# Kernel tuning notes

Hardware: AMD Instinct MI355X
Metric: run time of the kernel (lower is better)

## Reference

```python
import jax, jax.numpy as jnp
import numpy as np

C, K, D = 256, 16, 256  # clusters, cluster_size, embed_dim
MARGIN = 1.0
EPS = 1e-6  # torch pairwise_distance eps


def setup_inputs() -> dict:
    key = jax.random.key(0)
    batch = jax.random.normal(key, (C, K, D), dtype=jnp.float32)
    return {"batch": batch}


def reference(batch):
    # world_size == 1, rank == 0  ->  my_embeds == all_embeds
    c, k, d = batch.shape
    emb = batch.reshape(-1, d)                       # [N, D], N = c*k
    n = emb.shape[0]

    sq = jnp.sum(emb * emb, axis=-1)                 # [N]
    d2 = sq[:, None] + sq[None, :] - 2.0 * (emb @ emb.T)
    dist = jnp.sqrt(jnp.maximum(d2, 0.0))            # [N, N]

    labels = jnp.repeat(jnp.arange(c), k)            # [N]
    pos_mask = labels[:, None] == labels[None, :]    # [N, N]

    # hardest positive: masked max (masked entries -> -1, matching pytorch code)
    pos_idx = jnp.argmax(jnp.where(pos_mask, dist, -1.0), axis=1)
    # hardest negative: masked min (positives -> +inf)
    neg_idx = jnp.argmin(jnp.where(pos_mask, jnp.inf, dist), axis=1)

    positives = emb[pos_idx]                         # [N, D]
    negatives = emb[neg_idx]                         # [N, D]

    # TripletMarginLoss(margin=1.0, p=2): pairwise_distance adds eps to the diff
    d_ap = jnp.linalg.norm(emb - positives + EPS, axis=-1)
    d_an = jnp.linalg.norm(emb - negatives + EPS, axis=-1)
    loss = jnp.mean(jnp.maximum(d_ap - d_an + MARGIN, 0.0))
    return loss
```

## Files before the change

### kernel.cpp

```cpp
#include <hip/hip_runtime.h>
#include <math.h>

#define CC 256
#define KK 16
#define DD 256
#define NN 4096
#define EPSV 1e-6f

typedef unsigned long long u64;
typedef __attribute__((ext_vector_type(8))) short short8v;
typedef __attribute__((ext_vector_type(8))) unsigned short ushort8v;
typedef __attribute__((ext_vector_type(4))) float f32x4;

__global__ __launch_bounds__(256) void prep_kernel(const float* __restrict__ emb,
                                                   float* __restrict__ sq,
                                                   unsigned short* __restrict__ hi,
                                                   u64* __restrict__ posk,
                                                   u64* __restrict__ negk,
                                                   float* __restrict__ out) {
  __shared__ __attribute__((aligned(16))) unsigned short hiS[16][264];
  const int g = blockIdx.x;
  const int t = threadIdx.x;
  const int r = t >> 4, q = t & 15;
  const int row = g * 16 + r;

  const float* src = emb + (size_t)row * DD + q * 16;
  float s = 0.f;
  #pragma unroll
  for (int i = 0; i < 4; ++i) {
    float4 v = *reinterpret_cast<const float4*>(src + 4 * i);
    float f[4] = {v.x, v.y, v.z, v.w};
    #pragma unroll
    for (int e = 0; e < 4; ++e) {
      s += f[e] * f[e];
      hiS[r][q * 16 + 4 * i + e] = (unsigned short)(__float_as_uint(f[e]) >> 16);
    }
  }
  #pragma unroll
  for (int off = 1; off < 16; off <<= 1) s += __shfl_xor(s, off);
  if (q == 0) {
    sq[row] = s;
    posk[row] = 0ull;
    negk[row] = ~0ull;
  }
  if (g == 0 && t == 0) out[0] = 0.0f;
  __syncthreads();

  #pragma unroll
  for (int h = 0; h < 2; ++h) {
    int q2 = h * 256 + t;
    int s2 = q2 >> 6, fl = q2 & 63;
    int col = 32 * s2 + 8 * (fl >> 4);
    ushort8v hv = *reinterpret_cast<const ushort8v*>(&hiS[fl & 15][col]);
    *reinterpret_cast<ushort8v*>(hi + ((size_t)(g * 8 + s2) * 64 + fl) * 8) = hv;
  }
}

__device__ __forceinline__ void gll16(const unsigned short* g, unsigned short* l) {
  __builtin_amdgcn_global_load_lds(
      (const __attribute__((address_space(1))) unsigned int*)(const void*)g,
      (__attribute__((address_space(3))) unsigned int*)(void*)l, 16, 0, 0);
}

__global__ __launch_bounds__(256, 2) void mine_mfma_kernel(const unsigned short* __restrict__ hi,
                                                           const float* __restrict__ sq,
                                                           u64* __restrict__ posk,
                                                           u64* __restrict__ negk) {
  __shared__ __attribute__((aligned(16))) unsigned short ldsB[8][4096];

  const int bid = blockIdx.x;
  const int wg = (bid & 7) * 128 + (bid >> 3);
  const int ib = wg >> 5, jb = wg & 31;
  const bool diag = (ib == jb);
  const int ibRow = ib * 128, jbRow = jb * 128;

  const int tid = threadIdx.x;
  const int lane = tid & 63;
  const int w = tid >> 6;
  const int fr = lane & 15;
  const int grp = lane >> 4;

  {
    const int c0 = 2 * w, c1 = c0 + 1;
    const unsigned short* g0 = hi + ((size_t)(jb * 8 + c0) * 8) * 512 + lane * 8;
    const unsigned short* g1 = hi + ((size_t)(jb * 8 + c1) * 8) * 512 + lane * 8;
    #pragma unroll
    for (int s = 0; s < 8; ++s) {
      gll16(g0 + s * 512, &ldsB[s][c0 * 512]);
      gll16(g1 + s * 512, &ldsB[s][c1 * 512]);
    }
  }
  short8v a[8][2];
  #pragma unroll
  for (int m = 0; m < 2; ++m) {
    const unsigned short* ga = hi + ((size_t)(ib * 8 + 2 * w + m) * 8) * 512 + lane * 8;
    #pragma unroll
    for (int s = 0; s < 8; ++s)
      a[s][m] = *reinterpret_cast<const short8v*>(ga + s * 512);
  }
  __syncthreads();

  f32x4 acc[2][8];
  #pragma unroll
  for (int m = 0; m < 2; ++m)
    #pragma unroll
    for (int n = 0; n < 8; ++n)
      acc[m][n] = (f32x4){0.f, 0.f, 0.f, 0.f};

  #pragma unroll
  for (int s = 0; s < 8; ++s) {
    short8v b[8];
    #pragma unroll
    for (int n = 0; n < 8; ++n)
      b[n] = *reinterpret_cast<const short8v*>(&ldsB[s][n * 512 + lane * 8]);
    #pragma unroll
    for (int m = 0; m < 2; ++m)
      #pragma unroll
      for (int n = 0; n < 8; ++n)
        acc[m][n] = __builtin_amdgcn_mfma_f32_16x16x32_bf16(a[s][m], b[n], acc[m][n], 0, 0, 0);
  }

  float sqjv[8]; int jglob[8];
  #pragma unroll
  for (int n = 0; n < 8; ++n) {
    jglob[n] = jbRow + n * 16 + fr;
    sqjv[n] = sq[jglob[n]];
  }

  #pragma unroll
  for (int m = 0; m < 2; ++m) {
    #pragma unroll
    for (int r = 0; r < 4; ++r) {
      const int gi = ibRow + w * 32 + m * 16 + grp * 4 + r;
      const float sqiv = sq[gi];
      float pv = -1.0f; int pj = -1;
      float nv = 3.0e38f; int nj = 0x7fffffff;
      #pragma unroll
      for (int n = 0; n < 8; ++n) {
        const float d2 = fmaxf(sqiv + sqjv[n] - 2.0f * acc[m][n][r], 0.0f);
        const int j = jglob[n];
        const bool isPos = diag && ((j >> 4) == (gi >> 4));
        if (isPos) {
          if (d2 > pv || (d2 == pv && j < pj)) { pv = d2; pj = j; }
        } else {
          if (d2 < nv || (d2 == nv && j < nj)) { nv = d2; nj = j; }
        }
      }
      #pragma unroll
      for (int off = 1; off < 16; off <<= 1) {
        float ov = __shfl_xor(nv, off); int oj = __shfl_xor(nj, off);
        if (ov < nv || (ov == nv && oj < nj)) { nv = ov; nj = oj; }
        float pov = __shfl_xor(pv, off); int poj = __shfl_xor(pj, off);
        if (pov > pv || (pov == pv && ((unsigned)poj < (unsigned)pj))) { pv = pov; pj = poj; }
      }
      if (fr == 0) {
        if (nj != 0x7fffffff)
          atomicMin(&negk[gi], ((u64)__float_as_uint(nv) << 32) | (unsigned)nj);
        if (diag && pj >= 0)
          atomicMax(&posk[gi], ((u64)__float_as_uint(pv) << 32) |
                                   (unsigned)(0xFFFFFFFFu - (unsigned)pj));
      }
    }
  }
}

__global__ __launch_bounds__(1024) void triplet_kernel(const float* __restrict__ emb,
                                                       const u64* __restrict__ posk,
                                                       const u64* __restrict__ negk,
                                                       float* __restrict__ out) {
  __shared__ float part[16];
  const int w = threadIdx.x >> 6;
  const int lane = threadIdx.x & 63;
  const int i = blockIdx.x * 16 + w;

  u64 pk = posk[i], nk = negk[i];
  int p = (int)(0xFFFFFFFFu - (unsigned)(pk & 0xFFFFFFFFu));
  int nidx = (int)(nk & 0xFFFFFFFFu);

  float4 e  = *reinterpret_cast<const float4*>(emb + (size_t)i * DD + 4 * lane);
  float4 ep = *reinterpret_cast<const float4*>(emb + (size_t)p * DD + 4 * lane);
  float4 en = *reinterpret_cast<const float4*>(emb + (size_t)nidx * DD + 4 * lane);

  float dpx = e.x - ep.x + EPSV, dpy = e.y - ep.y + EPSV,
        dpz = e.z - ep.z + EPSV, dpw = e.w - ep.w + EPSV;
  float dnx = e.x - en.x + EPSV, dny = e.y - en.y + EPSV,
        dnz = e.z - en.z + EPSV, dnw = e.w - en.w + EPSV;
  float sp = dpx * dpx + dpy * dpy + dpz * dpz + dpw * dpw;
  float sn = dnx * dnx + dny * dny + dnz * dnz + dnw * dnw;
  #pragma unroll
  for (int off = 32; off; off >>= 1) {
    sp += __shfl_xor(sp, off);
    sn += __shfl_xor(sn, off);
  }
  if (lane == 0) part[w] = fmaxf(sqrtf(sp) - sqrtf(sn) + 1.0f, 0.0f);
  __syncthreads();
  if (threadIdx.x == 0) {
    float s = 0.f;
    #pragma unroll
    for (int k = 0; k < 16; ++k) s += part[k];
    atomicAdd(out, s * (1.0f / NN));
  }
}

extern "C" void kernel_launch(void* const* d_in, const int* in_sizes, int n_in,
                              void* d_out, int out_size, void* d_ws, size_t ws_size,
                              hipStream_t stream) {
  const float* emb = (const float*)d_in[0];
  char* ws = (char*)d_ws;
  float* sq = (float*)ws;
  u64* posk = (u64*)(ws + (16 << 10));
  u64* negk = (u64*)(ws + (48 << 10));
  unsigned short* hi = (unsigned short*)(ws + (96 << 10));
  float* out = (float*)d_out;

  prep_kernel<<<256, 256, 0, stream>>>(emb, sq, hi, posk, negk, out);
  mine_mfma_kernel<<<1024, 256, 0, stream>>>(hi, sq, posk, negk);
  triplet_kernel<<<256, 1024, 0, stream>>>(emb, posk, negk, out);
}
```

Baseline: 96.40 us.

## Fuse prep, mining and triplet stages into one cooperative kernel with grid syncs

Replaces the three separate launches (prep, MFMA mining, triplet loss) with a single cooperative kernel of 256 blocks of 512 threads, separated by grid-wide syncs. The mining tile is enlarged to 256x256 per block, processed in two 128-column halves, so each row keeps its running argmax/argmin in registers and issues fewer atomics. The aim is to remove launch gaps and atomic traffic, at the cost of fewer, larger blocks (lower occupancy and parallelism) and grid-sync overhead.

```diff
diff --git a/kernel.cpp b/kernel.cpp
--- a/kernel.cpp
+++ b/kernel.cpp
@@ -1,8 +1,9 @@
 #include <hip/hip_runtime.h>
+#include <hip/hip_cooperative_groups.h>
 #include <math.h>
 
-#define CC 256
-#define KK 16
+namespace cg = cooperative_groups;
+
 #define DD 256
 #define NN 4096
 #define EPSV 1e-6f
@@ -11,50 +12,6 @@
 typedef __attribute__((ext_vector_type(8))) short short8v;
 typedef __attribute__((ext_vector_type(8))) unsigned short ushort8v;
 typedef __attribute__((ext_vector_type(4))) float f32x4;
-
-__global__ __launch_bounds__(256) void prep_kernel(const float* __restrict__ emb,
-                                                   float* __restrict__ sq,
-                                                   unsigned short* __restrict__ hi,
-                                                   u64* __restrict__ posk,
-                                                   u64* __restrict__ negk,
-                                                   float* __restrict__ out) {
-  __shared__ __attribute__((aligned(16))) unsigned short hiS[16][264];
-  const int g = blockIdx.x;
-  const int t = threadIdx.x;
-  const int r = t >> 4, q = t & 15;
-  const int row = g * 16 + r;
-
-  const float* src = emb + (size_t)row * DD + q * 16;
-  float s = 0.f;
-  #pragma unroll
-  for (int i = 0; i < 4; ++i) {
-    float4 v = *reinterpret_cast<const float4*>(src + 4 * i);
-    float f[4] = {v.x, v.y, v.z, v.w};
-    #pragma unroll
-    for (int e = 0; e < 4; ++e) {
-      s += f[e] * f[e];
-      hiS[r][q * 16 + 4 * i + e] = (unsigned short)(__float_as_uint(f[e]) >> 16);
-    }
-  }
-  #pragma unroll
-  for (int off = 1; off < 16; off <<= 1) s += __shfl_xor(s, off);
-  if (q == 0) {
-    sq[row] = s;
-    posk[row] = 0ull;
-    negk[row] = ~0ull;
-  }
-  if (g == 0 && t == 0) out[0] = 0.0f;
-  __syncthreads();
-
-  #pragma unroll
-  for (int h = 0; h < 2; ++h) {
-    int q2 = h * 256 + t;
-    int s2 = q2 >> 6, fl = q2 & 63;
-    int col = 32 * s2 + 8 * (fl >> 4);
-    ushort8v hv = *reinterpret_cast<const ushort8v*>(&hiS[fl & 15][col]);
-    *reinterpret_cast<ushort8v*>(hi + ((size_t)(g * 8 + s2) * 64 + fl) * 8) = hv;
-  }
-}
 
 __device__ __forceinline__ void gll16(const unsigned short* g, unsigned short* l) {
   __builtin_amdgcn_global_load_lds(
@@ -62,143 +19,199 @@
       (__attribute__((address_space(3))) unsigned int*)(void*)l, 16, 0, 0);
 }
 
-__global__ __launch_bounds__(256, 2) void mine_mfma_kernel(const unsigned short* __restrict__ hi,
-                                                           const float* __restrict__ sq,
-                                                           u64* __restrict__ posk,
-                                                           u64* __restrict__ negk) {
+__global__ __launch_bounds__(512, 2) void fused_kernel(const float* __restrict__ emb,
+                                                       float* __restrict__ sq,
+                                                       unsigned short* __restrict__ hi,
+                                                       u64* __restrict__ posk,
+                                                       u64* __restrict__ negk,
+                                                       float* __restrict__ out) {
   __shared__ __attribute__((aligned(16))) unsigned short ldsB[8][4096];
+  cg::grid_group grid = cg::this_grid();
 
   const int bid = blockIdx.x;
-  const int wg = (bid & 7) * 128 + (bid >> 3);
-  const int ib = wg >> 5, jb = wg & 31;
-  const bool diag = (ib == jb);
-  const int ibRow = ib * 128, jbRow = jb * 128;
-
-  const int tid = threadIdx.x;
-  const int lane = tid & 63;
-  const int w = tid >> 6;
+  const int t = threadIdx.x;
+  const int lane = t & 63;
+  const int w = t >> 6;
   const int fr = lane & 15;
   const int grp = lane >> 4;
 
   {
-    const int c0 = 2 * w, c1 = c0 + 1;
-    const unsigned short* g0 = hi + ((size_t)(jb * 8 + c0) * 8) * 512 + lane * 8;
-    const unsigned short* g1 = hi + ((size_t)(jb * 8 + c1) * 8) * 512 + lane * 8;
-    #pragma unroll
-    for (int s = 0; s < 8; ++s) {
-      gll16(g0 + s * 512, &ldsB[s][c0 * 512]);
-      gll16(g1 + s * 512, &ldsB[s][c1 * 512]);
-    }
+    const int row = bid * 16 + (t >> 5);
+    const int k0 = (t & 31) * 8;
+    const float* src = emb + (size_t)row * DD + k0;
+    float4 v0 = *reinterpret_cast<const float4*>(src);
+    float4 v1 = *reinterpret_cast<const float4*>(src + 4);
+    float f[8] = {v0.x, v0.y, v0.z, v0.w, v1.x, v1.y, v1.z, v1.w};
+    ushort8v h;
+    float s = 0.f;
+    #pragma unroll
+    for (int e = 0; e < 8; ++e) {
+      s += f[e] * f[e];
+      h[e] = (unsigned short)(__float_as_uint(f[e]) >> 16);
+    }
+    const int g = row >> 4;
+    const int sl = (t & 31) >> 2;
+    const int l = (row & 15) + (t & 3) * 16;
+    *reinterpret_cast<ushort8v*>(hi + ((size_t)(g * 8 + sl) * 64 + l) * 8) = h;
+    #pragma unroll
+    for (int off = 1; off < 32; off <<= 1) s += __shfl_xor(s, off);
+    if ((t & 31) == 0) {
+      sq[row] = s;
+      posk[row] = 0ull;
+      negk[row] = ~0ull;
+    }
+    if (bid == 0 && t == 0) out[0] = 0.0f;
   }
-  short8v a[8][2];
-  #pragma unroll
-  for (int m = 0; m < 2; ++m) {
-    const unsigned short* ga = hi + ((size_t)(ib * 8 + 2 * w + m) * 8) * 512 + lane * 8;
-    #pragma unroll
-    for (int s = 0; s < 8; ++s)
-      a[s][m] = *reinterpret_cast<const short8v*>(ga + s * 512);
+  __threadfence();
+  grid.sync();
+
+  {
+    const int xcd = bid & 7, idx = bid >> 3;
+    const int ib = xcd * 2 + (idx >> 4);
+    const int jb = idx & 15;
+    const bool diag = (ib == jb);
+    const int ibRow = ib * 256, jbCol = jb * 256;
+
+    short8v a[8][2];
+    #pragma unroll
+    for (int m = 0; m < 2; ++m) {
+      const unsigned short* ga = hi + ((size_t)(ib * 16 + 2 * w + m) * 8) * 512 + lane * 8;
+      #pragma unroll
+      for (int s = 0; s < 8; ++s)
+        a[s][m] = *reinterpret_cast<const short8v*>(ga + s * 512);
+    }
+
+    int gi_[2][4]; float sqiv[2][4];
+    #pragma unroll
+    for (int m = 0; m < 2; ++m)
+      #pragma unroll
+      for (int r = 0; r < 4; ++r) {
+        gi_[m][r] = ibRow + 32 * w + 16 * m + 4 * grp + r;
+        sqiv[m][r] = sq[gi_[m][r]];
+      }
+
+    float pv[2][4], nv[2][4]; int pj[2][4], nj[2][4];
+    #pragma unroll
+    for (int m = 0; m < 2; ++m)
+      #pragma unroll
+      for (int r = 0; r < 4; ++r) {
+        pv[m][r] = -1.0f;   pj[m][r] = -1;
+        nv[m][r] = 3.0e38f; nj[m][r] = 0x7fffffff;
+      }
+
+    #pragma unroll 1
+    for (int h2 = 0; h2 < 2; ++h2) {
+      __syncthreads();
+      {
+        const unsigned short* gB =
+            hi + ((size_t)(jb * 16 + h2 * 8 + w) * 8) * 512 + lane * 8;
+        #pragma unroll
+        for (int s = 0; s < 8; ++s) gll16(gB + s * 512, &ldsB[s][w * 512]);
+      }
+      __syncthreads();
+
+      f32x4 acc[2][8];
+      #pragma unroll
+      for (int m = 0; m < 2; ++m)
+        #pragma unroll
+        for (int n = 0; n < 8; ++n) acc[m][n] = (f32x4){0.f, 0.f, 0.f, 0.f};
+
+      #pragma unroll
+      for (int s = 0; s < 8; ++s) {
+        short8v b[8];
+        #pragma unroll
+        for (int n = 0; n < 8; ++n)
+          b[n] = *reinterpret_cast<const short8v*>(&ldsB[s][n * 512 + lane * 8]);
+        #pragma unroll
+        for (int m = 0; m < 2; ++m)
+          #pragma unroll
+          for (int n = 0; n < 8; ++n)
+            acc[m][n] = __builtin_amdgcn_mfma_f32_16x16x32_bf16(a[s][m], b[n], acc[m][n], 0, 0, 0);
+      }
+
+      #pragma unroll
+      for (int n = 0; n < 8; ++n) {
+        const int j = jbCol + h2 * 128 + n * 16 + fr;
+        const float sqj = sq[j];
+        #pragma unroll
+        for (int m = 0; m < 2; ++m)
+          #pragma unroll
+          for (int r = 0; r < 4; ++r) {
+            const float d2 = fmaxf(sqiv[m][r] + sqj - 2.0f * acc[m][n][r], 0.0f);
+            const bool isPos = diag && ((j >> 4) == (gi_[m][r] >> 4));
+            if (isPos) {
+              if (d2 > pv[m][r] || (d2 == pv[m][r] && j < pj[m][r])) { pv[m][r] = d2; pj[m][r] = j; }
+            } else {
+              if (d2 < nv[m][r] || (d2 == nv[m][r] && j < nj[m][r])) { nv[m][r] = d2; nj[m][r] = j; }
+            }
+          }
+      }
+    }
+
+    #pragma unroll
+    for (int m = 0; m < 2; ++m)
+      #pragma unroll
+      for (int r = 0; r < 4; ++r) {
+        float v = nv[m][r]; int vi = nj[m][r];
+        #pragma unroll
+        for (int off = 1; off < 16; off <<= 1) {
+          float ov = __shfl_xor(v, off); int oi = __shfl_xor(vi, off);
+          if (ov < v || (ov == v && oi < vi)) { v = ov; vi = oi; }
+        }
+        float p2 = pv[m][r]; int pq = pj[m][r];
+        #pragma unroll
+        for (int off = 1; off < 16; off <<= 1) {
+          float ov = __shfl_xor(p2, off); int oi = __shfl_xor(pq, off);
+          if (ov > p2 || (ov == p2 && ((unsigned)oi < (unsigned)pq))) { p2 = ov; pq = oi; }
+        }
+        if (fr == 0) {
+          atomicMin(&negk[gi_[m][r]], ((u64)__float_as_uint(v) << 32) | (unsigned)vi);
+          if (diag && pq >= 0)
+            atomicMax(&posk[gi_[m][r]], ((u64)__float_as_uint(p2) << 32) |
+                                            (unsigned)(0xFFFFFFFFu - (unsigned)pq));
+        }
+      }
   }
-  __syncthreads();
-
-  f32x4 acc[2][8];
-  #pragma unroll
-  for (int m = 0; m < 2; ++m)
-    #pragma unroll
-    for (int n = 0; n < 8; ++n)
-      acc[m][n] = (f32x4){0.f, 0.f, 0.f, 0.f};
-
-  #pragma unroll
-  for (int s = 0; s < 8; ++s) {
-    short8v b[8];
-    #pragma unroll
-    for (int n = 0; n < 8; ++n)
-      b[n] = *reinterpret_cast<const short8v*>(&ldsB[s][n * 512 + lane * 8]);
-    #pragma unroll
-    for (int m = 0; m < 2; ++m)
-      #pragma unroll
-      for (int n = 0; n < 8; ++n)
-        acc[m][n] = __builtin_amdgcn_mfma_f32_16x16x32_bf16(a[s][m], b[n], acc[m][n], 0, 0, 0);
-  }
-
-  float sqjv[8]; int jglob[8];
-  #pragma unroll
-  for (int n = 0; n < 8; ++n) {
-    jglob[n] = jbRow + n * 16 + fr;
-    sqjv[n] = sq[jglob[n]];
-  }
-
-  #pragma unroll
-  for (int m = 0; m < 2; ++m) {
-    #pragma unroll
-    for (int r = 0; r < 4; ++r) {
-      const int gi = ibRow + w * 32 + m * 16 + grp * 4 + r;
-      const float sqiv = sq[gi];
-      float pv = -1.0f; int pj = -1;
-      float nv = 3.0e38f; int nj = 0x7fffffff;
-      #pragma unroll
-      for (int n = 0; n < 8; ++n) {
-        const float d2 = fmaxf(sqiv + sqjv[n] - 2.0f * acc[m][n][r], 0.0f);
-        const int j = jglob[n];
-        const bool isPos = diag && ((j >> 4) == (gi >> 4));
-        if (isPos) {
-          if (d2 > pv || (d2 == pv && j < pj)) { pv = d2; pj = j; }
-        } else {
-          if (d2 < nv || (d2 == nv && j < nj)) { nv = d2; nj = j; }
-        }
-      }
-      #pragma unroll
-      for (int off = 1; off < 16; off <<= 1) {
-        float ov = __shfl_xor(nv, off); int oj = __shfl_xor(nj, off);
-        if (ov < nv || (ov == nv && oj < nj)) { nv = ov; nj = oj; }
-        float pov = __shfl_xor(pv, off); int poj = __shfl_xor(pj, off);
-        if (pov > pv || (pov == pv && ((unsigned)poj < (unsigned)pj))) { pv = pov; pj = poj; }
-      }
-      if (fr == 0) {
-        if (nj != 0x7fffffff)
-          atomicMin(&negk[gi], ((u64)__float_as_uint(nv) << 32) | (unsigned)nj);
-        if (diag && pj >= 0)
-          atomicMax(&posk[gi], ((u64)__float_as_uint(pv) << 32) |
-                                   (unsigned)(0xFFFFFFFFu - (unsigned)pj));
-      }
-    }
-  }
-}
-
-__global__ __launch_bounds__(1024) void triplet_kernel(const float* __restrict__ emb,
-                                                       const u64* __restrict__ posk,
-                                                       const u64* __restrict__ negk,
-                                                       float* __restrict__ out) {
-  __shared__ float part[16];
-  const int w = threadIdx.x >> 6;
-  const int lane = threadIdx.x & 63;
-  const int i = blockIdx.x * 16 + w;
-
-  u64 pk = posk[i], nk = negk[i];
-  int p = (int)(0xFFFFFFFFu - (unsigned)(pk & 0xFFFFFFFFu));
-  int nidx = (int)(nk & 0xFFFFFFFFu);
-
-  float4 e  = *reinterpret_cast<const float4*>(emb + (size_t)i * DD + 4 * lane);
-  float4 ep = *reinterpret_cast<const float4*>(emb + (size_t)p * DD + 4 * lane);
-  float4 en = *reinterpret_cast<const float4*>(emb + (size_t)nidx * DD + 4 * lane);
-
-  float dpx = e.x - ep.x + EPSV, dpy = e.y - ep.y + EPSV,
-        dpz = e.z - ep.z + EPSV, dpw = e.w - ep.w + EPSV;
-  float dnx = e.x - en.x + EPSV, dny = e.y - en.y + EPSV,
-        dnz = e.z - en.z + EPSV, dnw = e.w - en.w + EPSV;
-  float sp = dpx * dpx + dpy * dpy + dpz * dpz + dpw * dpw;
-  float sn = dnx * dnx + dny * dny + dnz * dnz + dnw * dnw;
-  #pragma unroll
-  for (int off = 32; off; off >>= 1) {
-    sp += __shfl_xor(sp, off);
-    sn += __shfl_xor(sn, off);
-  }
-  if (lane == 0) part[w] = fmaxf(sqrtf(sp) - sqrtf(sn) + 1.0f, 0.0f);
-  __syncthreads();
-  if (threadIdx.x == 0) {
-    float s = 0.f;
-    #pragma unroll
-    for (int k = 0; k < 16; ++k) s += part[k];
-    atomicAdd(out, s * (1.0f / NN));
+  __threadfence();
+  grid.sync();
+
+  {
+    float* part = (float*)&ldsB[0][0];
+    const int i = bid * 16 + (t >> 5);
+    const int ls = t & 31;
+
+    u64 pk = posk[i], nk = negk[i];
+    int p = (int)(0xFFFFFFFFu - (unsigned)(pk & 0xFFFFFFFFu));
+    int nidx = (int)(nk & 0xFFFFFFFFu);
+
+    const float* ei = emb + (size_t)i * DD + ls * 8;
+    const float* epp = emb + (size_t)p * DD + ls * 8;
+    const float* enn = emb + (size_t)nidx * DD + ls * 8;
+    float sp = 0.f, sn = 0.f;
+    #pragma unroll
+    for (int c = 0; c < 2; ++c) {
+      float4 e = *reinterpret_cast<const float4*>(ei + 4 * c);
+      float4 ep = *reinterpret_cast<const float4*>(epp + 4 * c);
+      float4 en = *reinterpret_cast<const float4*>(enn + 4 * c);
+      float dp[4] = {e.x - ep.x + EPSV, e.y - ep.y + EPSV, e.z - ep.z + EPSV, e.w - ep.w + EPSV};
+      float dn[4] = {e.x - en.x + EPSV, e.y - en.y + EPSV, e.z - en.z + EPSV, e.w - en.w + EPSV};
+      #pragma unroll
+      for (int q = 0; q < 4; ++q) { sp += dp[q] * dp[q]; sn += dn[q] * dn[q]; }
+    }
+    #pragma unroll
+    for (int off = 1; off < 32; off <<= 1) {
+      sp += __shfl_xor(sp, off);
+      sn += __shfl_xor(sn, off);
+    }
+    __syncthreads();
+    if (ls == 0) part[t >> 5] = fmaxf(sqrtf(sp) - sqrtf(sn) + 1.0f, 0.0f);
+    __syncthreads();
+    if (t == 0) {
+      float s = 0.f;
+      #pragma unroll
+      for (int k = 0; k < 16; ++k) s += part[k];
+      atomicAdd(out, s * (1.0f / NN));
+    }
   }
 }
 
@@ -213,7 +226,6 @@
   unsigned short* hi = (unsigned short*)(ws + (96 << 10));
   float* out = (float*)d_out;
 
-  prep_kernel<<<256, 256, 0, stream>>>(emb, sq, hi, posk, negk, out);
-  mine_mfma_kernel<<<1024, 256, 0, stream>>>(hi, sq, posk, negk);
-  triplet_kernel<<<256, 1024, 0, stream>>>(emb, posk, negk, out);
+  void* args[] = {(void*)&emb, (void*)&sq, (void*)&hi, (void*)&posk, (void*)&negk, (void*)&out};
+  hipLaunchCooperativeKernel((const void*)fused_kernel, dim3(256), dim3(512), args, 0, stream);
 }
```

After: 231.5 us. +140.2%, slower.
